# Performance work log

Measured on AMD Instinct MI355X. Metric: run time of the kernel, lower is better.

## Reference

```python
import jax, jax.numpy as jnp
import numpy as np


def setup_inputs() -> dict:
    key = jax.random.key(0)
    k1, k2 = jax.random.split(key)
    batch, dim = 16384, 1024
    x = jax.random.normal(k1, (batch, dim), dtype=jnp.float32)
    centers = jax.random.uniform(k2, (dim, dim), dtype=jnp.float32)  # matches torch.rand init
    return {"x": x, "centers": centers}


def reference(x, centers):
    # Pairwise squared distance ||x_b - c_k||^2 via the expanded form
    # (avoids the O(batch*dim*dim) diff tensor the torch code materializes).
    x_sq = jnp.sum(x * x, axis=-1, keepdims=True)          # [B, 1]
    c_sq = jnp.sum(centers * centers, axis=-1)             # [K]
    cross = jnp.einsum('bd,kd->bk', x, centers)            # [B, K]
    dist_sq = x_sq - 2.0 * cross + c_sq                    # [B, K]
    # output = log(softmax(-0.5 * dist_sq)) -> numerically stable log-softmax
    return jax.nn.log_softmax(-0.5 * dist_sq, axis=-1)
```

## Files before the change

### kernel.cpp

```cpp
#include <hip/hip_runtime.h>
#include <math.h>

typedef __attribute__((ext_vector_type(8))) short short8;
typedef __attribute__((ext_vector_type(4))) float f32x4;

__device__ inline short f2bf(float f) {
    unsigned u = __float_as_uint(f);
    u += 0x7FFFu + ((u >> 16) & 1u);
    return (short)(u >> 16);
}

__global__ __launch_bounds__(128) void cast_centers_frag(const float* __restrict__ c,
                                                         short* __restrict__ cbF,
                                                         float* __restrict__ chalf, int K) {
    const int n = blockIdx.x;
    const int i = threadIdx.x;
    const int k0 = i * 8;
    const float* row = c + (size_t)n * K;
    float4 a = *(const float4*)(row + k0);
    float4 b = *(const float4*)(row + k0 + 4);
    float s = a.x * a.x + a.y * a.y + a.z * a.z + a.w * a.w +
              b.x * b.x + b.y * b.y + b.z * b.z + b.w * b.w;
    short8 o;
    o[0] = f2bf(a.x); o[1] = f2bf(a.y); o[2] = f2bf(a.z); o[3] = f2bf(a.w);
    o[4] = f2bf(b.x); o[5] = f2bf(b.y); o[6] = f2bf(b.z); o[7] = f2bf(b.w);
    const size_t slab = (size_t)(K / 16) * 1024;
    const size_t addr = (size_t)(k0 >> 5) * slab + (size_t)(n >> 4) * 1024 +
                        (size_t)((n & 15) + ((k0 >> 3) & 3) * 16) * 16;
    *(short8*)((char*)cbF + addr) = o;
#pragma unroll
    for (int off = 32; off; off >>= 1) s += __shfl_xor(s, off);
    __shared__ float red[2];
    if ((i & 63) == 0) red[i >> 6] = s;
    __syncthreads();
    if (i == 0) chalf[n] = 0.5f * (red[0] + red[1]);
}

#define SCR 16384

__global__ __launch_bounds__(512, 2) void fused_kernel(
    const float* __restrict__ x,
    const short* __restrict__ cbF,
    const float* __restrict__ chalf,
    float* __restrict__ out,
    int M, int N, int K) {
    __shared__ char lds[16384 + 4608];
    const int t = threadIdx.x;
    const int l = t & 63, w = t >> 6, lr = l & 15, hi = l >> 4;
    const int brow = blockIdx.x * 64;

    const char* bbase = (const char*)cbF + w * 8192 + l * 16;

    const int ar = t >> 3, c8 = t & 7;
    const float* xsrc = x + (size_t)(brow + ar) * K + c8 * 4;
    const int awofs = (ar >> 4) * 1024 + (ar & 15) * 16 + (c8 >> 1) * 256 + (c8 & 1) * 8;

#define LDB(dst, ks) do { _Pragma("unroll")                                      \
    for (int j = 0; j < 8; ++j)                                                  \
        dst[j] = *(const short8*)(bbase + (size_t)(ks) * 65536 + j * 1024); } while (0)

#define AW(ks, fv) do {                                                          \
    short4 p_;                                                                   \
    p_.x = f2bf((fv).x); p_.y = f2bf((fv).y);                                    \
    p_.z = f2bf((fv).z); p_.w = f2bf((fv).w);                                    \
    *(short4*)(lds + ((ks) & 3) * 4096 + awofs) = p_; } while (0)

    f32x4 acc[4][8];
#pragma unroll
    for (int m = 0; m < 4; ++m)
#pragma unroll
        for (int n = 0; n < 8; ++n)
#pragma unroll
            for (int q = 0; q < 4; ++q) acc[m][n][q] = 0.f;

    short8 Ba[8], Bb[8];
    float4 xf0, xf1;

    xf0 = *(const float4*)(xsrc);
    xf1 = *(const float4*)(xsrc + 32);
    LDB(Ba, 0);
    AW(0, xf0);
    AW(1, xf1);
    xf0 = *(const float4*)(xsrc + 64);
    xf1 = *(const float4*)(xsrc + 96);
    LDB(Bb, 1);
    asm volatile("s_waitcnt lgkmcnt(0)" ::: "memory");
    __builtin_amdgcn_s_barrier();

#define MFMACL(Bcur) do {                                                        \
    __builtin_amdgcn_s_setprio(1);                                               \
    _Pragma("unroll")                                                            \
    for (int m = 0; m < 4; ++m)                                                  \
        _Pragma("unroll")                                                        \
        for (int n = 0; n < 8; ++n)                                              \
            acc[m][n] = __builtin_amdgcn_mfma_f32_16x16x32_bf16(af[m], Bcur[n],  \
                                                                acc[m][n], 0, 0, 0); \
    __builtin_amdgcn_s_setprio(0); } while (0)

#define AREAD(ks) short8 af[4];                                                  \
    _Pragma("unroll")                                                            \
    for (int m = 0; m < 4; ++m)                                                  \
        af[m] = *(const short8*)(lds + ((ks) & 3) * 4096 + m * 1024 + l * 16);

#define SYNCP() do {                                                             \
    asm volatile("s_waitcnt lgkmcnt(0)" ::: "memory");                           \
    __builtin_amdgcn_s_barrier();                                                \
    __builtin_amdgcn_sched_barrier(0); } while (0)

    for (int ks = 0; ks < 28; ks += 2) {
        {
            AREAD(ks); SYNCP();
            MFMACL(Ba);
            AW(ks + 2, xf0);
            LDB(Ba, ks + 2);
            xf0 = *(const float4*)(xsrc + (size_t)(ks + 4) * 32);
        }
        {
            AREAD(ks + 1); SYNCP();
            MFMACL(Bb);
            AW(ks + 3, xf1);
            LDB(Bb, ks + 3);
            xf1 = *(const float4*)(xsrc + (size_t)(ks + 5) * 32);
        }
    }
    { AREAD(28); SYNCP(); MFMACL(Ba); AW(30, xf0); LDB(Ba, 30); }
    { AREAD(29); SYNCP(); MFMACL(Bb); AW(31, xf1); LDB(Bb, 31); }
    { AREAD(30); SYNCP(); MFMACL(Ba); }
    { AREAD(31); SYNCP(); MFMACL(Bb); }
#undef AREAD
#undef MFMACL
#undef SYNCP
#undef LDB
#undef AW

    float ch[8];
#pragma unroll
    for (int n = 0; n < 8; ++n) ch[n] = chalf[w * 128 + n * 16 + lr];

    float pm[4][4];
#pragma unroll
    for (int m = 0; m < 4; ++m)
#pragma unroll
        for (int q = 0; q < 4; ++q) {
            float v = acc[m][0][q] - ch[0];
#pragma unroll
            for (int n = 1; n < 8; ++n) v = fmaxf(v, acc[m][n][q] - ch[n]);
            pm[m][q] = v;
        }
#pragma unroll
    for (int d = 1; d <= 8; d <<= 1)
#pragma unroll
        for (int m = 0; m < 4; ++m)
#pragma unroll
            for (int q = 0; q < 4; ++q) pm[m][q] = fmaxf(pm[m][q], __shfl_xor(pm[m][q], d));
    if (lr == 0) {
#pragma unroll
        for (int m = 0; m < 4; ++m)
#pragma unroll
            for (int q = 0; q < 4; ++q)
                *(float*)(lds + SCR + (m * 16 + hi * 4 + q) * 32 + w * 4) = pm[m][q];
    }
    __syncthreads();
    if (t < 64) {
        float4 a = *(const float4*)(lds + SCR + t * 32);
        float4 b = *(const float4*)(lds + SCR + t * 32 + 16);
        float g = fmaxf(fmaxf(fmaxf(a.x, a.y), fmaxf(a.z, a.w)),
                        fmaxf(fmaxf(b.x, b.y), fmaxf(b.z, b.w)));
        *(float*)(lds + SCR + 4096 + t * 4) = g;
    }
    __syncthreads();

    float ps[4][4];
#pragma unroll
    for (int m = 0; m < 4; ++m)
#pragma unroll
        for (int q = 0; q < 4; ++q) {
            const float g = *(const float*)(lds + SCR + 4096 + (m * 16 + hi * 4 + q) * 4);
            float s = 0.f;
#pragma unroll
            for (int n = 0; n < 8; ++n) s += __expf(acc[m][n][q] - ch[n] - g);
            ps[m][q] = s;
        }
#pragma unroll
    for (int d = 1; d <= 8; d <<= 1)
#pragma unroll
        for (int m = 0; m < 4; ++m)
#pragma unroll
            for (int q = 0; q < 4; ++q) ps[m][q] += __shfl_xor(ps[m][q], d);
    if (lr == 0) {
#pragma unroll
        for (int m = 0; m < 4; ++m)
#pragma unroll
            for (int q = 0; q < 4; ++q)
                *(float*)(lds + SCR + 2048 + (m * 16 + hi * 4 + q) * 32 + w * 4) = ps[m][q];
    }
    __syncthreads();
    if (t < 64) {
        float4 a = *(const float4*)(lds + SCR + 2048 + t * 32);
        float4 b = *(const float4*)(lds + SCR + 2048 + t * 32 + 16);
        float s = (a.x + a.y + a.z + a.w) + (b.x + b.y + b.z + b.w);
        *(float*)(lds + SCR + 4352 + t * 4) =
            *(const float*)(lds + SCR + 4096 + t * 4) + __logf(s);
    }
    __syncthreads();

#pragma unroll
    for (int m = 0; m < 4; ++m)
#pragma unroll
        for (int q = 0; q < 4; ++q) {
            const int R = m * 16 + hi * 4 + q;
            const float lse = *(const float*)(lds + SCR + 4352 + R * 4);
            float* orow = out + (size_t)(brow + R) * N + w * 128 + lr;
#pragma unroll
            for (int n = 0; n < 8; ++n)
                orow[n * 16] = acc[m][n][q] - ch[n] - lse;
        }
}

extern "C" void kernel_launch(void* const* d_in, const int* in_sizes, int n_in,
                              void* d_out, int out_size, void* d_ws, size_t ws_size,
                              hipStream_t stream) {
    const float* x = (const float*)d_in[0];
    const float* c = (const float*)d_in[1];
    float* out = (float*)d_out;

    int dim = (int)(sqrt((double)in_sizes[1]) + 0.5);
    int batch = in_sizes[0] / dim;

    size_t cb_bytes = (size_t)dim * dim * 2;
    short* cbF = (short*)d_ws;
    float* chalf = (float*)((char*)d_ws + cb_bytes);

    cast_centers_frag<<<dim, 128, 0, stream>>>(c, cbF, chalf, dim);

    fused_kernel<<<batch / 64, 512, 0, stream>>>(x, cbF, chalf, out, batch, dim, dim);
}
```

Before: 55.39 us.

## Split each 64-row block across 16 waves with half the columns per wave

Launches 1024-thread blocks where each of 16 waves owns 64 output columns instead of 128. This halves per-wave accumulators and B-fragment registers, and the A-tile staging, cross-wave max/sum reductions and output indexing are remapped to match. The goal is more waves in flight per CU to hide memory latency, traded against one block per CU, heavier barriers across 16 waves and reduced per-wave B reuse.

```diff
diff --git a/kernel.cpp b/kernel.cpp
--- a/kernel.cpp
+++ b/kernel.cpp
@@ -38,7 +38,7 @@
 
 #define SCR 16384
 
-__global__ __launch_bounds__(512, 2) void fused_kernel(
+__global__ __launch_bounds__(1024, 1) void fused_kernel(
     const float* __restrict__ x,
     const short* __restrict__ cbF,
     const float* __restrict__ chalf,
@@ -49,40 +49,39 @@
     const int l = t & 63, w = t >> 6, lr = l & 15, hi = l >> 4;
     const int brow = blockIdx.x * 64;
 
-    const char* bbase = (const char*)cbF + w * 8192 + l * 16;
-
-    const int ar = t >> 3, c8 = t & 7;
-    const float* xsrc = x + (size_t)(brow + ar) * K + c8 * 4;
-    const int awofs = (ar >> 4) * 1024 + (ar & 15) * 16 + (c8 >> 1) * 256 + (c8 & 1) * 8;
+    const char* bbase = (const char*)cbF + w * 4096 + l * 16;
+
+    const int ar = t >> 4, kp = t & 15;
+    const float* xsrc = x + (size_t)(brow + ar) * K + kp * 2;
+    const int awofs = (ar >> 4) * 1024 + ((ar & 15) + (kp >> 2) * 16) * 16 + (kp & 3) * 4;
 
 #define LDB(dst, ks) do { _Pragma("unroll")                                      \
-    for (int j = 0; j < 8; ++j)                                                  \
+    for (int j = 0; j < 4; ++j)                                                  \
         dst[j] = *(const short8*)(bbase + (size_t)(ks) * 65536 + j * 1024); } while (0)
 
-#define AW(ks, fv) do {                                                          \
-    short4 p_;                                                                   \
-    p_.x = f2bf((fv).x); p_.y = f2bf((fv).y);                                    \
-    p_.z = f2bf((fv).z); p_.w = f2bf((fv).w);                                    \
-    *(short4*)(lds + ((ks) & 3) * 4096 + awofs) = p_; } while (0)
-
-    f32x4 acc[4][8];
-#pragma unroll
-    for (int m = 0; m < 4; ++m)
-#pragma unroll
-        for (int n = 0; n < 8; ++n)
+#define AW(slot, fv) do {                                                        \
+    unsigned p_ = ((unsigned)(unsigned short)f2bf((fv).y) << 16) |               \
+                  (unsigned)(unsigned short)f2bf((fv).x);                        \
+    *(unsigned*)(lds + ((slot) & 3) * 4096 + awofs) = p_; } while (0)
+
+    f32x4 acc[4][4];
+#pragma unroll
+    for (int m = 0; m < 4; ++m)
+#pragma unroll
+        for (int n = 0; n < 4; ++n)
 #pragma unroll
             for (int q = 0; q < 4; ++q) acc[m][n][q] = 0.f;
 
-    short8 Ba[8], Bb[8];
-    float4 xf0, xf1;
-
-    xf0 = *(const float4*)(xsrc);
-    xf1 = *(const float4*)(xsrc + 32);
+    short8 Ba[4], Bb[4];
+    float2 xf0, xf1;
+
+    xf0 = *(const float2*)(xsrc);
+    xf1 = *(const float2*)(xsrc + 32);
     LDB(Ba, 0);
     AW(0, xf0);
     AW(1, xf1);
-    xf0 = *(const float4*)(xsrc + 64);
-    xf1 = *(const float4*)(xsrc + 96);
+    xf0 = *(const float2*)(xsrc + 64);
+    xf1 = *(const float2*)(xsrc + 96);
     LDB(Bb, 1);
     asm volatile("s_waitcnt lgkmcnt(0)" ::: "memory");
     __builtin_amdgcn_s_barrier();
@@ -92,15 +91,15 @@
     _Pragma("unroll")                                                            \
     for (int m = 0; m < 4; ++m)                                                  \
         _Pragma("unroll")                                                        \
-        for (int n = 0; n < 8; ++n)                                              \
+        for (int n = 0; n < 4; ++n)                                              \
             acc[m][n] = __builtin_amdgcn_mfma_f32_16x16x32_bf16(af[m], Bcur[n],  \
                                                                 acc[m][n], 0, 0, 0); \
     __builtin_amdgcn_s_setprio(0); } while (0)
 
-#define AREAD(ks) short8 af[4];                                                  \
+#define AREAD(slot) short8 af[4];                                                \
     _Pragma("unroll")                                                            \
     for (int m = 0; m < 4; ++m)                                                  \
-        af[m] = *(const short8*)(lds + ((ks) & 3) * 4096 + m * 1024 + l * 16);
+        af[m] = *(const short8*)(lds + ((slot) & 3) * 4096 + m * 1024 + l * 16);
 
 #define SYNCP() do {                                                             \
     asm volatile("s_waitcnt lgkmcnt(0)" ::: "memory");                           \
@@ -113,14 +112,14 @@
             MFMACL(Ba);
             AW(ks + 2, xf0);
             LDB(Ba, ks + 2);
-            xf0 = *(const float4*)(xsrc + (size_t)(ks + 4) * 32);
+            xf0 = *(const float2*)(xsrc + (size_t)(ks + 4) * 32);
         }
         {
             AREAD(ks + 1); SYNCP();
             MFMACL(Bb);
             AW(ks + 3, xf1);
             LDB(Bb, ks + 3);
-            xf1 = *(const float4*)(xsrc + (size_t)(ks + 5) * 32);
+            xf1 = *(const float2*)(xsrc + (size_t)(ks + 5) * 32);
         }
     }
     { AREAD(28); SYNCP(); MFMACL(Ba); AW(30, xf0); LDB(Ba, 30); }
@@ -133,9 +132,9 @@
 #undef LDB
 #undef AW
 
-    float ch[8];
-#pragma unroll
-    for (int n = 0; n < 8; ++n) ch[n] = chalf[w * 128 + n * 16 + lr];
+    float ch[4];
+#pragma unroll
+    for (int n = 0; n < 4; ++n) ch[n] = chalf[w * 64 + n * 16 + lr];
 
     float pm[4][4];
 #pragma unroll
@@ -144,7 +143,7 @@
         for (int q = 0; q < 4; ++q) {
             float v = acc[m][0][q] - ch[0];
 #pragma unroll
-            for (int n = 1; n < 8; ++n) v = fmaxf(v, acc[m][n][q] - ch[n]);
+            for (int n = 1; n < 4; ++n) v = fmaxf(v, acc[m][n][q] - ch[n]);
             pm[m][q] = v;
         }
 #pragma unroll
@@ -158,14 +157,16 @@
         for (int m = 0; m < 4; ++m)
 #pragma unroll
             for (int q = 0; q < 4; ++q)
-                *(float*)(lds + SCR + (m * 16 + hi * 4 + q) * 32 + w * 4) = pm[m][q];
+                *(float*)(lds + SCR + (m * 16 + hi * 4 + q) * 64 + w * 4) = pm[m][q];
     }
     __syncthreads();
     if (t < 64) {
-        float4 a = *(const float4*)(lds + SCR + t * 32);
-        float4 b = *(const float4*)(lds + SCR + t * 32 + 16);
-        float g = fmaxf(fmaxf(fmaxf(a.x, a.y), fmaxf(a.z, a.w)),
-                        fmaxf(fmaxf(b.x, b.y), fmaxf(b.z, b.w)));
+        float g = -1e30f;
+#pragma unroll
+        for (int j = 0; j < 4; ++j) {
+            float4 a = *(const float4*)(lds + SCR + t * 64 + j * 16);
+            g = fmaxf(g, fmaxf(fmaxf(a.x, a.y), fmaxf(a.z, a.w)));
+        }
         *(float*)(lds + SCR + 4096 + t * 4) = g;
     }
     __syncthreads();
@@ -178,7 +179,7 @@
             const float g = *(const float*)(lds + SCR + 4096 + (m * 16 + hi * 4 + q) * 4);
             float s = 0.f;
 #pragma unroll
-            for (int n = 0; n < 8; ++n) s += __expf(acc[m][n][q] - ch[n] - g);
+            for (int n = 0; n < 4; ++n) s += __expf(acc[m][n][q] - ch[n] - g);
             ps[m][q] = s;
         }
 #pragma unroll
@@ -192,13 +193,16 @@
         for (int m = 0; m < 4; ++m)
 #pragma unroll
             for (int q = 0; q < 4; ++q)
-                *(float*)(lds + SCR + 2048 + (m * 16 + hi * 4 + q) * 32 + w * 4) = ps[m][q];
+                *(float*)(lds + SCR + (m * 16 + hi * 4 + q) * 64 + w * 4) = ps[m][q];
     }
     __syncthreads();
     if (t < 64) {
-        float4 a = *(const float4*)(lds + SCR + 2048 + t * 32);
-        float4 b = *(const float4*)(lds + SCR + 2048 + t * 32 + 16);
-        float s = (a.x + a.y + a.z + a.w) + (b.x + b.y + b.z + b.w);
+        float s = 0.f;
+#pragma unroll
+        for (int j = 0; j < 4; ++j) {
+            float4 a = *(const float4*)(lds + SCR + t * 64 + j * 16);
+            s += a.x + a.y + a.z + a.w;
+        }
         *(float*)(lds + SCR + 4352 + t * 4) =
             *(const float*)(lds + SCR + 4096 + t * 4) + __logf(s);
     }
@@ -210,9 +214,9 @@
         for (int q = 0; q < 4; ++q) {
             const int R = m * 16 + hi * 4 + q;
             const float lse = *(const float*)(lds + SCR + 4352 + R * 4);
-            float* orow = out + (size_t)(brow + R) * N + w * 128 + lr;
-#pragma unroll
-            for (int n = 0; n < 8; ++n)
+            float* orow = out + (size_t)(brow + R) * N + w * 64 + lr;
+#pragma unroll
+            for (int n = 0; n < 4; ++n)
                 orow[n * 16] = acc[m][n][q] - ch[n] - lse;
         }
 }
@@ -233,5 +237,5 @@
 
     cast_centers_frag<<<dim, 128, 0, stream>>>(c, cbF, chalf, dim);
 
-    fused_kernel<<<batch / 64, 512, 0, stream>>>(x, cbF, chalf, out, batch, dim, dim);
-}
+    fused_kernel<<<batch / 64, 1024, 0, stream>>>(x, cbF, chalf, out, batch, dim, dim);
+}
```

Measured after the change: 56.83 us. +2.6%, slower.
